# Optimization experiments

Measured on AMD Instinct MI355X. Metric: run time of the kernel, lower is better.

Reference implementation:

```python
import jax, jax.numpy as jnp
import numpy as np

NC = 10   # num_classes
H = 6     # num_heads
C = 384   # dim
HD = C // H
B = 16    # batch (non-anchor rows)
T = 197   # tokens (1 cls + 196 image)
N = T - 1
SCALE = HD ** -0.5


def _ln(x, g, b):
    mu = jnp.mean(x, -1, keepdims=True)
    var = jnp.mean(jnp.square(x - mu), -1, keepdims=True)
    return (x - mu) * jax.lax.rsqrt(var + 1e-5) * g + b


def setup_inputs() -> dict:
    key = jax.random.key(0)
    ks = jax.random.split(key, 12)
    def w(k, shape):
        return jax.random.normal(k, shape, jnp.float32) * 0.02
    return {
        "x": jax.random.normal(ks[0], (B + NC, T, C), jnp.float32),
        "Wqv": w(ks[1], (C, 2 * C)),
        "Wk": w(ks[2], (C, C)),
        "Wq_proj": w(ks[3], (C, C)), "bq_proj": jnp.zeros((C,), jnp.float32),
        "Wqk": w(ks[4], (C, C)), "Wqk2": w(ks[5], (C, C)), "Wv": w(ks[6], (C, C)),
        "Wr_proj": w(ks[7], (C, C)), "br_proj": jnp.zeros((C,), jnp.float32),
        "g1": jnp.ones((C,), jnp.float32), "b1": jnp.zeros((C,), jnp.float32),
        "g2": jnp.ones((C,), jnp.float32), "b2": jnp.zeros((C,), jnp.float32),
        "g3": jnp.ones((C,), jnp.float32), "b3": jnp.zeros((C,), jnp.float32),
        "W1": w(ks[8], (C, 4 * C)), "bm1": jnp.zeros((4 * C,), jnp.float32),
        "W2": w(ks[9], (4 * C, C)), "bm2": jnp.zeros((C,), jnp.float32),
    }


def reference(x, Wqv, Wk, Wq_proj, bq_proj, Wqk, Wqk2, Wv, Wr_proj, br_proj,
              g1, b1, g2, b2, g3, b3, W1, bm1, W2, bm2):
    xs, anchors = x[:-NC], jax.lax.stop_gradient(x[-NC:])  # anchors .detach()
    x_im, a_im = xs[:, 1:], anchors[:, 1:]                  # [B,N,C], [NC,N,C]
    x_cls, a_cls = xs[:, :1], anchors[:, :1]                # [B,1,C], [NC,1,C]

    # ---- Quoter ----
    n1x = _ln(x_cls, g1, b1)[:, 0]    # [B,C]
    n1a = _ln(a_cls, g1, b1)[:, 0]    # [NC,C]
    qv = (n1a @ Wqv).reshape(NC, 2, H, HD)
    q, v = qv[:, 0], qv[:, 1]                       # [NC,H,HD]
    k = (n1x @ Wk).reshape(B, H, HD)                # [B,H,HD]
    attn_cls = jax.nn.softmax(jnp.einsum('nhd,bhd->bnh', q, k) * SCALE, axis=1)  # [B,NC,H]
    cls_out = jnp.einsum('bnh,nhd->bhd', attn_cls, v).reshape(B, 1, C) @ Wq_proj + bq_proj

    # ---- Rectifier ----
    n2x = _ln(x_im, g2, b2)   # [B,N,C]
    n2a = _ln(a_im, g2, b2)   # [NC,N,C]
    def heads(t, W):
        return (t @ W).reshape(t.shape[0], N, H, HD).transpose(0, 2, 1, 3)
    vr = heads(n2x, Wv)        # [B,H,N,HD]
    qh = heads(n2x, Wqk)       # [B,H,N,HD]
    kh = heads(n2a, Wqk)       # [NC,H,N,HD]
    q2 = heads(n2x, Wqk2)
    k2 = heads(n2a, Wqk2)
    # left_attn = relu(-(q @ k^T) * scale), right_attn = relu((k2 @ q2^T) * scale)
    left = jax.nn.relu(-SCALE * jnp.einsum('bhnd,chmd->bchnm', qh, kh))    # [B,NC,H,N,N]
    right = jax.nn.relu(SCALE * jnp.einsum('chmd,bhnd->bchmn', k2, q2))    # [B,NC,H,N,N]
    attn = jnp.einsum('bchnm,bchmk->bchnk', left, right).transpose(0, 2, 3, 1, 4)  # [B,H,N,NC,N]
    # faithful raw reshape [B,NC,H] -> [B,H,NC] (memory reinterpretation as in torch source)
    w2 = attn_cls.reshape(B, H, NC)
    tmp = jnp.einsum('bhc,bhnck->bhnk', w2, attn)                           # [B,H,N,N]
    # faithful raw reshape [B,H,N,HD] -> [B,N,C]
    rect = jnp.einsum('bhnk,bhkd->bhnd', tmp, vr).reshape(B, N, C) @ Wr_proj + br_proj

    x_im = x_im + rect
    xx = jnp.concatenate([cls_out, x_im], axis=1)        # [B,T,C]
    hdn = _ln(xx, g3, b3)
    xx = xx + (jax.nn.gelu(hdn @ W1 + bm1, approximate=False) @ W2 + bm2)
    return jnp.concatenate([xx, anchors], axis=0)        # [B+NC,T,C]
```

## Files before the change

### kernel.cpp

```cpp
#include <hip/hip_runtime.h>
#include <hip/hip_bf16.h>
#include <math.h>

#define SCL 0.125f

typedef float f32x4 __attribute__((ext_vector_type(4)));
typedef short bf16x8 __attribute__((ext_vector_type(8)));
#define MFMA16(a, b, c) __builtin_amdgcn_mfma_f32_16x16x32_bf16((a), (b), (c), 0, 0, 0)

__device__ __forceinline__ unsigned short f2bf(float f) {
    unsigned int u = __builtin_bit_cast(unsigned int, f);
    u = (u + 0x7FFFu + ((u >> 16) & 1u)) >> 16;
    return (unsigned short)u;
}

__device__ __forceinline__ float gelu_exact(float v) {
    return 0.5f * v * (1.f + erff(v * 0.70710678118654752f));
}

template <int BF16OUT>
__global__ void ln_kernel(const float* __restrict__ x, void* __restrict__ outp,
                          const float* __restrict__ g, const float* __restrict__ bt,
                          int mode) {
    const int row = blockIdx.x;
    const int lane = threadIdx.x;
    const float* src;
    if (mode == 0)      src = x + (size_t)row * (197 * 384);
    else if (mode == 4) {
        if (row < 3136) { int b = row / 196, n = row % 196; src = x + (size_t)(b * 197 + 1 + n) * 384; }
        else { int rr = row - 3136; int b = rr / 196, n = rr % 196; src = x + (size_t)((16 + b) * 197 + 1 + n) * 384; }
    }
    else                src = x + (size_t)row * 384;

    float v[6];
    float s = 0.f, s2 = 0.f;
#pragma unroll
    for (int j = 0; j < 6; j++) {
        v[j] = src[lane + j * 64];
        s += v[j];
        s2 += v[j] * v[j];
    }
#pragma unroll
    for (int o = 32; o; o >>= 1) {
        s  += __shfl_xor(s, o);
        s2 += __shfl_xor(s2, o);
    }
    const float mu = s * (1.f / 384.f);
    const float var = s2 * (1.f / 384.f) - mu * mu;
    const float rs = 1.f / sqrtf(var + 1e-5f);
#pragma unroll
    for (int j = 0; j < 6; j++) {
        const int c = lane + j * 64;
        const float r = (v[j] - mu) * rs * g[c] + bt[c];
        if (BF16OUT) ((unsigned short*)outp)[(size_t)row * 384 + c] = f2bf(r);
        else         ((float*)outp)[(size_t)row * 384 + c] = r;
    }
}

template <int M>
__global__ void gemm_cls(const float* __restrict__ A, const float* __restrict__ B,
                         const float* __restrict__ bias, float* __restrict__ C,
                         int N, int ldc) {
    __shared__ float sA[M * 384];
    __shared__ float red[4][M][64];
    const int t = threadIdx.x;
    const int tc = t & 63, ks = t >> 6;
    const int n = blockIdx.x * 64 + tc;
    for (int e = t; e < M * 384; e += 256) sA[e] = A[e];
    __syncthreads();
    float acc[M];
#pragma unroll
    for (int m = 0; m < M; m++) acc[m] = 0.f;
    const int k0 = ks * 96;
#pragma unroll 4
    for (int k = k0; k < k0 + 96; k++) {
        const float bv = B[(size_t)k * N + n];
#pragma unroll
        for (int m = 0; m < M; m++) acc[m] += sA[m * 384 + k] * bv;
    }
#pragma unroll
    for (int m = 0; m < M; m++) red[ks][m][tc] = acc[m];
    __syncthreads();
    if (ks == 0) {
#pragma unroll
        for (int m = 0; m < M; m++) {
            float s = red[0][m][tc] + red[1][m][tc] + red[2][m][tc] + red[3][m][tc];
            if (bias) s += bias[n];
            C[(size_t)m * ldc + n] = s;
        }
    }
}

__global__ void attn_cls_kernel(const float* __restrict__ qv, const float* __restrict__ kcls,
                                float* __restrict__ aflat, float* __restrict__ cls_pre) {
    const int b = blockIdx.x;
    const int t = threadIdx.x;
    __shared__ float kb[384];
    __shared__ float pl[60];
#pragma unroll
    for (int j = 0; j < 6; j++) kb[t + j * 64] = kcls[b * 384 + t + j * 64];
    __syncthreads();
    if (t < 60) {
        const int n = t / 6, h = t % 6;
        float acc = 0.f;
        for (int d = 0; d < 64; d++) acc += qv[n * 768 + h * 64 + d] * kb[h * 64 + d];
        pl[t] = acc * SCL;
    }
    __syncthreads();
    if (t < 6) {
        float m = -1e30f;
        for (int n = 0; n < 10; n++) m = fmaxf(m, pl[n * 6 + t]);
        float p[10], sum = 0.f;
        for (int n = 0; n < 10; n++) { p[n] = expf(pl[n * 6 + t] - m); sum += p[n]; }
        const float inv = 1.f / sum;
        for (int n = 0; n < 10; n++) {
            const float pr = p[n] * inv;
            pl[n * 6 + t] = pr;
            aflat[b * 60 + n * 6 + t] = pr;
        }
    }
    __syncthreads();
#pragma unroll
    for (int j = 0; j < 6; j++) {
        const int c = t + j * 64;
        const int h = c >> 6;
        float acc = 0.f;
        for (int n = 0; n < 10; n++) acc += pl[n * 6 + h] * qv[n * 768 + 384 + c];
        cls_pre[b * 384 + c] = acc;
    }
}

__global__ void wcast_t(const float* __restrict__ W, unsigned short* __restrict__ Wt,
                        int K, int N) {
    const int n0 = blockIdx.x * 64, k0 = blockIdx.y * 64;
    __shared__ unsigned short sT[64][72];
    const int t = threadIdx.x;
    for (int e = t; e < 4096; e += 256) {
        const int k = e >> 6, n = e & 63;
        sT[n][k] = f2bf(W[(size_t)(k0 + k) * N + n0 + n]);
    }
    __syncthreads();
    for (int e = t; e < 512; e += 256) {
        const int n = e >> 3, ch = e & 7;
        *(uint4*)&Wt[(size_t)(n0 + n) * K + k0 + ch * 8] = *(uint4*)&sT[n][ch * 8];
    }
}

__global__ void wcast3(const float* __restrict__ Wa, const float* __restrict__ Wb,
                       const float* __restrict__ Wc, unsigned short* __restrict__ Wt) {
    const float* W = blockIdx.z == 0 ? Wa : (blockIdx.z == 1 ? Wb : Wc);
    unsigned short* dst = Wt + (size_t)blockIdx.z * 384 * 384;
    const int n0 = blockIdx.x * 64, k0 = blockIdx.y * 64;
    __shared__ unsigned short sT[64][72];
    const int t = threadIdx.x;
    for (int e = t; e < 4096; e += 256) {
        const int k = e >> 6, n = e & 63;
        sT[n][k] = f2bf(W[(size_t)(k0 + k) * 384 + n0 + n]);
    }
    __syncthreads();
    for (int e = t; e < 512; e += 256) {
        const int n = e >> 3, ch = e & 7;
        *(uint4*)&dst[(size_t)(n0 + n) * 384 + k0 + ch * 8] = *(uint4*)&sT[n][ch * 8];
    }
}

template <int EPI>
__launch_bounds__(256)
__global__ void gemm_mfma(const unsigned short* __restrict__ A,
                          const unsigned short* __restrict__ Bt,
                          const float* __restrict__ bias, const float* __restrict__ res,
                          void* __restrict__ Cout, int M, int N, int K) {
    const int m0 = blockIdx.y * 64, n0 = blockIdx.x * 128;
    const int t = threadIdx.x;
    const int w = t >> 6, l = t & 63;
    const int lr = l & 15, lk = l >> 4;
    const int wr = w >> 1, wc = w & 1;

    __shared__ unsigned short sA[64][72];
    __shared__ unsigned short sB[128][72];

    f32x4 acc[2][4];
#pragma unroll
    for (int mi = 0; mi < 2; mi++)
#pragma unroll
        for (int nj = 0; nj < 4; nj++) acc[mi][nj] = (f32x4){0.f, 0.f, 0.f, 0.f};

    for (int k0 = 0; k0 < K; k0 += 64) {
        for (int e = t; e < 512; e += 256) {
            const int r = e >> 3, ch = e & 7;
            uint4 v = make_uint4(0, 0, 0, 0);
            const int row = m0 + r;
            if (row < M) v = *(const uint4*)(A + (size_t)row * K + k0 + ch * 8);
            *(uint4*)&sA[r][ch * 8] = v;
        }
        for (int e = t; e < 1024; e += 256) {
            const int r = e >> 3, ch = e & 7;
            *(uint4*)&sB[r][ch * 8] = *(const uint4*)(Bt + (size_t)(n0 + r) * K + k0 + ch * 8);
        }
        __syncthreads();
#pragma unroll
        for (int kc = 0; kc < 2; kc++) {
            bf16x8 af[2], bfr[4];
#pragma unroll
            for (int mi = 0; mi < 2; mi++)
                af[mi] = *(const bf16x8*)&sA[wr * 32 + mi * 16 + lr][kc * 32 + lk * 8];
#pragma unroll
            for (int nj = 0; nj < 4; nj++)
                bfr[nj] = *(const bf16x8*)&sB[wc * 64 + nj * 16 + lr][kc * 32 + lk * 8];
#pragma unroll
            for (int mi = 0; mi < 2; mi++)
#pragma unroll
                for (int nj = 0; nj < 4; nj++)
                    acc[mi][nj] = MFMA16(af[mi], bfr[nj], acc[mi][nj]);
        }
        __syncthreads();
    }

#pragma unroll
    for (int mi = 0; mi < 2; mi++)
#pragma unroll
        for (int nj = 0; nj < 4; nj++) {
            const int col = n0 + wc * 64 + nj * 16 + lr;
#pragma unroll
            for (int i = 0; i < 4; i++) {
                const int row = m0 + wr * 32 + mi * 16 + lk * 4 + i;
                if (row >= M) continue;
                float v = acc[mi][nj][i];
                if (EPI == 0) {
                    ((unsigned short*)Cout)[(size_t)row * N + col] = f2bf(v);
                } else if (EPI == 1) {
                    const int crow = row + row / 196 + 1;
                    v += bias[col] + res[(size_t)crow * N + col];
                    ((float*)Cout)[(size_t)crow * N + col] = v;
                } else if (EPI == 2) {
                    ((unsigned short*)Cout)[(size_t)row * N + col] = f2bf(gelu_exact(v + bias[col]));
                } else {
                    v += bias[col] + res[(size_t)row * N + col];
                    ((float*)Cout)[(size_t)row * N + col] = v;
                }
            }
        }
}

__global__ __launch_bounds__(256, 2)
void rz_kernel(const unsigned short* __restrict__ Q2b, const unsigned short* __restrict__ K2b,
               const unsigned short* __restrict__ VRb, unsigned short* __restrict__ Zt,
               int sq, int sk, int sv) {
    const int c = blockIdx.x, h = blockIdx.y, b = blockIdx.z;
    const int t = threadIdx.x;
    const int w = t >> 6, l = t & 63;
    const int lr = l & 15, lk = l >> 4;

    __shared__ unsigned short sVT[64 * 232];
    __shared__ unsigned short sR[4 * 16 * 232];
    unsigned short* sRw = sR + w * (16 * 232);

    const unsigned short* vrsrc = VRb + (size_t)(b * 196) * sv + h * 64;
    for (int e = t; e < 196 * 8; e += 256) {
        const int kk = e >> 3, ch = e & 7;
        uint4 v = *(const uint4*)(vrsrc + (size_t)kk * sv + ch * 8);
        unsigned short vs[8]; *(uint4*)vs = v;
#pragma unroll
        for (int j = 0; j < 8; j++) sVT[(ch * 8 + j) * 232 + kk] = vs[j];
    }
    for (int e = t; e < 64 * 36; e += 256) sVT[(e / 36) * 232 + 196 + (e % 36)] = 0;
    for (int e = l; e < 16 * 24; e += 64) sRw[(e / 24) * 232 + 208 + (e % 24)] = 0;

    bf16x8 qf0[13], qf1[13];
    const unsigned short* q2src = Q2b + (size_t)(b * 196) * sq + h * 64;
#pragma unroll
    for (int kt = 0; kt < 13; kt++) {
        const int r = kt * 16 + lr;
        if (r < 196) {
            const unsigned short* p = q2src + (size_t)r * sq;
            qf0[kt] = *(const bf16x8*)(p + lk * 8);
            qf1[kt] = *(const bf16x8*)(p + 32 + lk * 8);
        } else {
            qf0[kt] = (bf16x8){0, 0, 0, 0, 0, 0, 0, 0};
            qf1[kt] = (bf16x8){0, 0, 0, 0, 0, 0, 0, 0};
        }
    }
    __syncthreads();

    const unsigned short* k2src = K2b + (size_t)(c * 196) * sk + h * 64;
    unsigned short* zdst = Zt + ((((size_t)(b * 6 + h)) * 10 + c) * 64) * 208;

    for (int mt = w; mt < 13; mt += 4) {
        bf16x8 a0, a1;
        const int ar = mt * 16 + lr;
        if (ar < 196) {
            const unsigned short* p = k2src + (size_t)ar * sk;
            a0 = *(const bf16x8*)(p + lk * 8);
            a1 = *(const bf16x8*)(p + 32 + lk * 8);
        } else {
            a0 = (bf16x8){0, 0, 0, 0, 0, 0, 0, 0};
            a1 = (bf16x8){0, 0, 0, 0, 0, 0, 0, 0};
        }
#pragma unroll
        for (int kt = 0; kt < 13; kt++) {
            f32x4 acc = {0.f, 0.f, 0.f, 0.f};
            acc = MFMA16(a0, qf0[kt], acc);
            acc = MFMA16(a1, qf1[kt], acc);
#pragma unroll
            for (int i = 0; i < 4; i++)
                sRw[(lk * 4 + i) * 232 + kt * 16 + lr] = f2bf(fmaxf(0.f, SCL * acc[i]));
        }
#pragma unroll
        for (int dt = 0; dt < 4; dt++) {
            f32x4 acc = {0.f, 0.f, 0.f, 0.f};
#pragma unroll
            for (int kc = 0; kc < 7; kc++) {
                bf16x8 a  = *(const bf16x8*)&sRw[lr * 232 + kc * 32 + lk * 8];
                bf16x8 bb = *(const bf16x8*)&sVT[(dt * 16 + lr) * 232 + kc * 32 + lk * 8];
                acc = MFMA16(a, bb, acc);
            }
            unsigned short p[4];
#pragma unroll
            for (int i = 0; i < 4; i++) p[i] = f2bf(acc[i]);
            *(uint2*)&zdst[(size_t)(dt * 16 + lr) * 208 + mt * 16 + lk * 4] = *(uint2*)p;
        }
    }
}

__global__ __launch_bounds__(256)
void yz_kernel(const unsigned short* __restrict__ QHb, const unsigned short* __restrict__ KHb,
               const unsigned short* __restrict__ Zt, const float* __restrict__ aflat,
               unsigned short* __restrict__ rect) {
    const int ns = blockIdx.x, h = blockIdx.y, b = blockIdx.z;
    const int n0 = ns * 49;
    const int t = threadIdx.x;
    const int w = t >> 6, l = t & 63;
    const int lr = l & 15, lk = l >> 4;

    __shared__ unsigned short sKH[112 * 72];
    __shared__ unsigned short sZT[64 * 232];
    __shared__ unsigned short sL[64 * 232];

    for (int e = t; e < 64 * 24; e += 256) {
        sZT[(e / 24) * 232 + 208 + (e % 24)] = 0;
        sL [(e / 24) * 232 + 208 + (e % 24)] = 0;
    }

    bf16x8 qf[2];
    {
        const int rel = w * 16 + lr;
        if (rel < 49) {
            const unsigned short* qsrc = QHb + (size_t)(b * 196 + n0 + rel) * 1152 + h * 64;
            qf[0] = *(const bf16x8*)(qsrc + lk * 8);
            qf[1] = *(const bf16x8*)(qsrc + 32 + lk * 8);
        } else {
            qf[0] = (bf16x8){0, 0, 0, 0, 0, 0, 0, 0};
            qf[1] = (bf16x8){0, 0, 0, 0, 0, 0, 0, 0};
        }
    }

    f32x4 y[4];
#pragma unroll
    for (int i = 0; i < 4; i++) y[i] = (f32x4){0.f, 0.f, 0.f, 0.f};
    __syncthreads();

    for (int c = 0; c < 10; c++) {
        const unsigned short* zsrc = Zt + ((((size_t)(b * 6 + h)) * 10 + c) * 64) * 208;
        for (int e = t; e < 64 * 26; e += 256) {
            const int d = e / 26, mc = e % 26;
            *(uint4*)&sZT[d * 232 + mc * 8] = *(const uint4*)(zsrc + (size_t)d * 208 + mc * 8);
        }
        for (int e = t; e < 112 * 8; e += 256) {
            const int r = e >> 3, ch = e & 7;
            *(uint4*)&sKH[r * 72 + ch * 8] =
                *(const uint4*)(KHb + (size_t)(c * 196 + r) * 768 + h * 64 + ch * 8);
        }
        const float wc = aflat[b * 60 + h * 10 + c];
        __syncthreads();
#pragma unroll
        for (int mt = 0; mt < 7; mt++) {
            f32x4 acc = {0.f, 0.f, 0.f, 0.f};
            bf16x8 b0 = *(const bf16x8*)&sKH[(mt * 16 + lr) * 72 + lk * 8];
            acc = MFMA16(qf[0], b0, acc);
            bf16x8 b1 = *(const bf16x8*)&sKH[(mt * 16 + lr) * 72 + 32 + lk * 8];
            acc = MFMA16(qf[1], b1, acc);
            const int lrow = w * 16 + lk * 4, lcol = mt * 16 + lr;
#pragma unroll
            for (int i = 0; i < 4; i++)
                sL[(lrow + i) * 232 + lcol] = f2bf(wc * fmaxf(0.f, -SCL * acc[i]));
        }
        __syncthreads();
        for (int e = t; e < 96 * 8; e += 256) {
            const int r = e >> 3, ch = e & 7;
            uint4 v = make_uint4(0, 0, 0, 0);
            if (112 + r < 196)
                v = *(const uint4*)(KHb + (size_t)(c * 196 + 112 + r) * 768 + h * 64 + ch * 8);
            *(uint4*)&sKH[r * 72 + ch * 8] = v;
        }
        __syncthreads();
#pragma unroll
        for (int mt = 7; mt < 13; mt++) {
            f32x4 acc = {0.f, 0.f, 0.f, 0.f};
            bf16x8 b0 = *(const bf16x8*)&sKH[((mt - 7) * 16 + lr) * 72 + lk * 8];
            acc = MFMA16(qf[0], b0, acc);
            bf16x8 b1 = *(const bf16x8*)&sKH[((mt - 7) * 16 + lr) * 72 + 32 + lk * 8];
            acc = MFMA16(qf[1], b1, acc);
            const int lrow = w * 16 + lk * 4, lcol = mt * 16 + lr;
#pragma unroll
            for (int i = 0; i < 4; i++)
                sL[(lrow + i) * 232 + lcol] = f2bf(wc * fmaxf(0.f, -SCL * acc[i]));
        }
#pragma unroll
        for (int dt = 0; dt < 4; dt++) {
            f32x4 acc = y[dt];
#pragma unroll
            for (int mc = 0; mc < 7; mc++) {
                bf16x8 a  = *(const bf16x8*)&sL[(w * 16 + lr) * 232 + mc * 32 + lk * 8];
                bf16x8 bb = *(const bf16x8*)&sZT[(dt * 16 + lr) * 232 + mc * 32 + lk * 8];
                acc = MFMA16(a, bb, acc);
            }
            y[dt] = acc;
        }
        __syncthreads();
    }

#pragma unroll
    for (int dt = 0; dt < 4; dt++)
#pragma unroll
        for (int i = 0; i < 4; i++) {
            const int rel = w * 16 + lk * 4 + i;
            if (rel < 49)
                rect[(((size_t)(b * 6 + h)) * 196 + n0 + rel) * 64 + dt * 16 + lr] = f2bf(y[dt][i]);
        }
}

__global__ void copy_anchors(const float* __restrict__ x, float* __restrict__ out) {
    const int e = blockIdx.x * 256 + threadIdx.x;
    if (e < 189120) {
        const int base = 16 * 197 * 384 / 4;
        ((float4*)out)[base + e] = ((const float4*)x)[base + e];
    }
}

extern "C" void kernel_launch(void* const* d_in, const int* in_sizes, int n_in,
                              void* d_out, int out_size, void* d_ws, size_t ws_size,
                              hipStream_t stream) {
    (void)in_sizes; (void)n_in; (void)out_size; (void)ws_size;
    const float* x       = (const float*)d_in[0];
    const float* Wqv     = (const float*)d_in[1];
    const float* Wk      = (const float*)d_in[2];
    const float* Wq_proj = (const float*)d_in[3];
    const float* bq_proj = (const float*)d_in[4];
    const float* Wqk     = (const float*)d_in[5];
    const float* Wqk2    = (const float*)d_in[6];
    const float* Wv      = (const float*)d_in[7];
    const float* Wr_proj = (const float*)d_in[8];
    const float* br_proj = (const float*)d_in[9];
    const float* g1      = (const float*)d_in[10];
    const float* b1      = (const float*)d_in[11];
    const float* g2      = (const float*)d_in[12];
    const float* b2      = (const float*)d_in[13];
    const float* g3      = (const float*)d_in[14];
    const float* b3      = (const float*)d_in[15];
    const float* W1      = (const float*)d_in[16];
    const float* bm1     = (const float*)d_in[17];
    const float* W2      = (const float*)d_in[18];
    const float* bm2     = (const float*)d_in[19];

    float* ws = (float*)d_ws;
    float* n1      = ws;
    float* qv      = ws + 9984;
    float* kcls    = ws + 17664;
    float* aflat   = ws + 23808;
    float* cls_pre = ws + 24768;
    unsigned short* n2x_bf  = (unsigned short*)(ws + 30912);
    unsigned short* n2a_bf  = (unsigned short*)(ws + 633024);
    unsigned short* Px      = (unsigned short*)(ws + 1009344);
    unsigned short* Pa      = (unsigned short*)(ws + 2815680);
    unsigned short* rect_bf = (unsigned short*)(ws + 3568320);
    float* xx               = ws + 4170432;
    unsigned short* Wx_t    = (unsigned short*)(ws + 5380800);
    unsigned short* Wr_t    = (unsigned short*)(ws + 5601984);
    unsigned short* W1_t    = (unsigned short*)(ws + 5675712);
    unsigned short* W2_t    = (unsigned short*)(ws + 5970624);
    unsigned short* Zt      = (unsigned short*)(ws + 6265536);
    unsigned short* hdn_bf  = (unsigned short*)(ws + 6265536);
    unsigned short* G_bf    = (unsigned short*)(ws + 6870720);
    float* outf = (float*)d_out;

    unsigned short* QHb = Px;
    unsigned short* Q2b = Px + 384;
    unsigned short* VRb = Px + 768;
    unsigned short* KHb = Pa;
    unsigned short* K2b = Pa + 384;

    wcast3<<<dim3(6, 6, 3), 256, 0, stream>>>(Wqk, Wqk2, Wv, Wx_t);
    wcast_t<<<dim3(6, 6),  256, 0, stream>>>(Wr_proj, Wr_t, 384, 384);
    wcast_t<<<dim3(24, 6), 256, 0, stream>>>(W1, W1_t, 384, 1536);
    wcast_t<<<dim3(6, 24), 256, 0, stream>>>(W2, W2_t, 1536, 384);
    ln_kernel<0><<<26, 64, 0, stream>>>(x, n1, g1, b1, 0);
    gemm_cls<10><<<12, 256, 0, stream>>>(n1 + 16 * 384, Wqv, nullptr, qv, 768, 768);
    gemm_cls<16><<<6, 256, 0, stream>>>(n1, Wk, nullptr, kcls, 384, 384);
    attn_cls_kernel<<<16, 64, 0, stream>>>(qv, kcls, aflat, cls_pre);
    ln_kernel<1><<<5096, 64, 0, stream>>>(x, n2x_bf, g2, b2, 4);
    gemm_mfma<0><<<dim3(9, 49), 256, 0, stream>>>(n2x_bf, Wx_t, nullptr, nullptr, Px, 3136, 1152, 384);
    gemm_mfma<0><<<dim3(6, 31), 256, 0, stream>>>(n2a_bf, Wx_t, nullptr, nullptr, Pa, 1960, 768, 384);
    rz_kernel<<<dim3(10, 6, 16), 256, 0, stream>>>(Q2b, K2b, VRb, Zt, 1152, 768, 1152);
    yz_kernel<<<dim3(4, 6, 16), 256, 0, stream>>>(QHb, KHb, Zt, aflat, rect_bf);
    gemm_cls<16><<<6, 256, 0, stream>>>(cls_pre, Wq_proj, bq_proj, xx, 384, 197 * 384);
    gemm_mfma<1><<<dim3(3, 49), 256, 0, stream>>>(rect_bf, Wr_t, br_proj, x, xx, 3136, 384, 384);
    ln_kernel<1><<<3152, 64, 0, stream>>>(xx, hdn_bf, g3, b3, 3);
    gemm_mfma<2><<<dim3(12, 50), 256, 0, stream>>>(hdn_bf, W1_t, bm1, nullptr, G_bf, 3152, 1536, 384);
    gemm_mfma<3><<<dim3(3, 50), 256, 0, stream>>>(G_bf, W2_t, bm2, xx, outf, 3152, 384, 1536);
    copy_anchors<<<739, 256, 0, stream>>>(x, outf);
}
```

Measured before the change: 470.1 us.

## Merge weight-cast and layernorm launches; prefetch next-class tiles in yz_kernel

Four weight-cast launches are merged into one flattened grid, and the two first-stage layernorms are merged into a single launch, cutting per-launch overhead. In yz_kernel, the Z and KH tiles for the next class are loaded into registers while the current class computes, a software-pipelining step meant to hide global-memory latency. It also adds an occupancy hint of 2 blocks per SM. The prefetch registers raise register pressure, which may conflict with that occupancy target and cause spills.

```diff
diff --git a/kernel.cpp b/kernel.cpp
--- a/kernel.cpp
+++ b/kernel.cpp
@@ -18,19 +18,23 @@
     return 0.5f * v * (1.f + erff(v * 0.70710678118654752f));
 }
 
-template <int BF16OUT>
-__global__ void ln_kernel(const float* __restrict__ x, void* __restrict__ outp,
-                          const float* __restrict__ g, const float* __restrict__ bt,
-                          int mode) {
+__global__ void ln_all(const float* __restrict__ x, float* __restrict__ n1,
+                       unsigned short* __restrict__ n2_bf,
+                       const float* __restrict__ g1, const float* __restrict__ b1,
+                       const float* __restrict__ g2, const float* __restrict__ b2) {
     const int row = blockIdx.x;
     const int lane = threadIdx.x;
     const float* src;
-    if (mode == 0)      src = x + (size_t)row * (197 * 384);
-    else if (mode == 4) {
-        if (row < 3136) { int b = row / 196, n = row % 196; src = x + (size_t)(b * 197 + 1 + n) * 384; }
-        else { int rr = row - 3136; int b = rr / 196, n = rr % 196; src = x + (size_t)((16 + b) * 197 + 1 + n) * 384; }
-    }
-    else                src = x + (size_t)row * 384;
+    const float *g, *bt;
+    if (row < 26) {
+        src = x + (size_t)row * (197 * 384);
+        g = g1; bt = b1;
+    } else {
+        const int rr = row - 26;
+        if (rr < 3136) { int b = rr / 196, n = rr % 196; src = x + (size_t)(b * 197 + 1 + n) * 384; }
+        else { int r2 = rr - 3136; int b = r2 / 196, n = r2 % 196; src = x + (size_t)((16 + b) * 197 + 1 + n) * 384; }
+        g = g2; bt = b2;
+    }
 
     float v[6];
     float s = 0.f, s2 = 0.f;
@@ -52,8 +56,36 @@
     for (int j = 0; j < 6; j++) {
         const int c = lane + j * 64;
         const float r = (v[j] - mu) * rs * g[c] + bt[c];
-        if (BF16OUT) ((unsigned short*)outp)[(size_t)row * 384 + c] = f2bf(r);
-        else         ((float*)outp)[(size_t)row * 384 + c] = r;
+        if (row < 26) n1[(size_t)row * 384 + c] = r;
+        else          n2_bf[(size_t)(row - 26) * 384 + c] = f2bf(r);
+    }
+}
+
+__global__ void ln3_kernel(const float* __restrict__ x, unsigned short* __restrict__ outp,
+                           const float* __restrict__ g, const float* __restrict__ bt) {
+    const int row = blockIdx.x;
+    const int lane = threadIdx.x;
+    const float* src = x + (size_t)row * 384;
+    float v[6];
+    float s = 0.f, s2 = 0.f;
+#pragma unroll
+    for (int j = 0; j < 6; j++) {
+        v[j] = src[lane + j * 64];
+        s += v[j];
+        s2 += v[j] * v[j];
+    }
+#pragma unroll
+    for (int o = 32; o; o >>= 1) {
+        s  += __shfl_xor(s, o);
+        s2 += __shfl_xor(s2, o);
+    }
+    const float mu = s * (1.f / 384.f);
+    const float var = s2 * (1.f / 384.f) - mu * mu;
+    const float rs = 1.f / sqrtf(var + 1e-5f);
+#pragma unroll
+    for (int j = 0; j < 6; j++) {
+        const int c = lane + j * 64;
+        outp[(size_t)row * 384 + c] = f2bf((v[j] - mu) * rs * g[c] + bt[c]);
     }
 }
 
@@ -130,9 +162,29 @@
     }
 }
 
-__global__ void wcast_t(const float* __restrict__ W, unsigned short* __restrict__ Wt,
-                        int K, int N) {
-    const int n0 = blockIdx.x * 64, k0 = blockIdx.y * 64;
+__global__ void wcast_all(const float* __restrict__ Wqk, const float* __restrict__ Wqk2,
+                          const float* __restrict__ Wv, const float* __restrict__ Wr,
+                          const float* __restrict__ W1, const float* __restrict__ W2,
+                          unsigned short* __restrict__ Wx_t, unsigned short* __restrict__ Wr_t,
+                          unsigned short* __restrict__ W1_t, unsigned short* __restrict__ W2_t) {
+    const int bid = blockIdx.x;
+    const float* W; unsigned short* dst; int K, N, nx, ky;
+    if (bid < 108) {
+        const int z = bid / 36, rem = bid % 36;
+        W = (z == 0) ? Wqk : (z == 1 ? Wqk2 : Wv);
+        dst = Wx_t + (size_t)z * 384 * 384;
+        K = 384; N = 384; nx = rem % 6; ky = rem / 6;
+    } else if (bid < 144) {
+        const int rem = bid - 108;
+        W = Wr; dst = Wr_t; K = 384; N = 384; nx = rem % 6; ky = rem / 6;
+    } else if (bid < 288) {
+        const int rem = bid - 144;
+        W = W1; dst = W1_t; K = 384; N = 1536; nx = rem % 24; ky = rem / 24;
+    } else {
+        const int rem = bid - 288;
+        W = W2; dst = W2_t; K = 1536; N = 384; nx = rem % 6; ky = rem / 6;
+    }
+    const int n0 = nx * 64, k0 = ky * 64;
     __shared__ unsigned short sT[64][72];
     const int t = threadIdx.x;
     for (int e = t; e < 4096; e += 256) {
@@ -142,25 +194,7 @@
     __syncthreads();
     for (int e = t; e < 512; e += 256) {
         const int n = e >> 3, ch = e & 7;
-        *(uint4*)&Wt[(size_t)(n0 + n) * K + k0 + ch * 8] = *(uint4*)&sT[n][ch * 8];
-    }
-}
-
-__global__ void wcast3(const float* __restrict__ Wa, const float* __restrict__ Wb,
-                       const float* __restrict__ Wc, unsigned short* __restrict__ Wt) {
-    const float* W = blockIdx.z == 0 ? Wa : (blockIdx.z == 1 ? Wb : Wc);
-    unsigned short* dst = Wt + (size_t)blockIdx.z * 384 * 384;
-    const int n0 = blockIdx.x * 64, k0 = blockIdx.y * 64;
-    __shared__ unsigned short sT[64][72];
-    const int t = threadIdx.x;
-    for (int e = t; e < 4096; e += 256) {
-        const int k = e >> 6, n = e & 63;
-        sT[n][k] = f2bf(W[(size_t)(k0 + k) * 384 + n0 + n]);
-    }
-    __syncthreads();
-    for (int e = t; e < 512; e += 256) {
-        const int n = e >> 3, ch = e & 7;
-        *(uint4*)&dst[(size_t)(n0 + n) * 384 + k0 + ch * 8] = *(uint4*)&sT[n][ch * 8];
+        *(uint4*)&dst[(size_t)(n0 + n) * K + k0 + ch * 8] = *(uint4*)&sT[n][ch * 8];
     }
 }
 
@@ -322,7 +356,7 @@
     }
 }
 
-__global__ __launch_bounds__(256)
+__global__ __launch_bounds__(256, 2)
 void yz_kernel(const unsigned short* __restrict__ QHb, const unsigned short* __restrict__ KHb,
                const unsigned short* __restrict__ Zt, const float* __restrict__ aflat,
                unsigned short* __restrict__ rect) {
@@ -354,24 +388,69 @@
         }
     }
 
+    const size_t zbase = (((size_t)(b * 6 + h)) * 10) * 64 * 208;
+
+    uint4 zt_r[7], kh1_r[4], kh2_r[3];
+
+    {
+        const unsigned short* zsrc = Zt + zbase;
+#pragma unroll
+        for (int i = 0; i < 7; i++) {
+            const int e = t + i * 256;
+            if (e < 1664) { const int d = e / 26, mc = e % 26;
+                zt_r[i] = *(const uint4*)(zsrc + (size_t)d * 208 + mc * 8); }
+        }
+#pragma unroll
+        for (int i = 0; i < 4; i++) {
+            const int e = t + i * 256;
+            if (e < 896) { const int r = e >> 3, ch = e & 7;
+                kh1_r[i] = *(const uint4*)(KHb + (size_t)r * 768 + h * 64 + ch * 8); }
+        }
+    }
+
     f32x4 y[4];
 #pragma unroll
     for (int i = 0; i < 4; i++) y[i] = (f32x4){0.f, 0.f, 0.f, 0.f};
     __syncthreads();
 
     for (int c = 0; c < 10; c++) {
-        const unsigned short* zsrc = Zt + ((((size_t)(b * 6 + h)) * 10 + c) * 64) * 208;
-        for (int e = t; e < 64 * 26; e += 256) {
-            const int d = e / 26, mc = e % 26;
-            *(uint4*)&sZT[d * 232 + mc * 8] = *(const uint4*)(zsrc + (size_t)d * 208 + mc * 8);
-        }
-        for (int e = t; e < 112 * 8; e += 256) {
+#pragma unroll
+        for (int i = 0; i < 7; i++) {
+            const int e = t + i * 256;
+            if (e < 1664) { const int d = e / 26, mc = e % 26;
+                *(uint4*)&sZT[d * 232 + mc * 8] = zt_r[i]; }
+        }
+#pragma unroll
+        for (int i = 0; i < 4; i++) {
+            const int e = t + i * 256;
+            if (e < 896) { const int r = e >> 3, ch = e & 7;
+                *(uint4*)&sKH[r * 72 + ch * 8] = kh1_r[i]; }
+        }
+#pragma unroll
+        for (int i = 0; i < 3; i++) {
+            const int e = t + i * 256;
             const int r = e >> 3, ch = e & 7;
-            *(uint4*)&sKH[r * 72 + ch * 8] =
-                *(const uint4*)(KHb + (size_t)(c * 196 + r) * 768 + h * 64 + ch * 8);
+            kh2_r[i] = (112 + r < 196)
+                ? *(const uint4*)(KHb + (size_t)(c * 196 + 112 + r) * 768 + h * 64 + ch * 8)
+                : make_uint4(0, 0, 0, 0);
         }
         const float wc = aflat[b * 60 + h * 10 + c];
         __syncthreads();
+        if (c < 9) {
+            const unsigned short* zsrc = Zt + zbase + (size_t)(c + 1) * 64 * 208;
+#pragma unroll
+            for (int i = 0; i < 7; i++) {
+                const int e = t + i * 256;
+                if (e < 1664) { const int d = e / 26, mc = e % 26;
+                    zt_r[i] = *(const uint4*)(zsrc + (size_t)d * 208 + mc * 8); }
+            }
+#pragma unroll
+            for (int i = 0; i < 4; i++) {
+                const int e = t + i * 256;
+                if (e < 896) { const int r = e >> 3, ch = e & 7;
+                    kh1_r[i] = *(const uint4*)(KHb + (size_t)((c + 1) * 196 + r) * 768 + h * 64 + ch * 8); }
+            }
+        }
 #pragma unroll
         for (int mt = 0; mt < 7; mt++) {
             f32x4 acc = {0.f, 0.f, 0.f, 0.f};
@@ -385,12 +464,11 @@
                 sL[(lrow + i) * 232 + lcol] = f2bf(wc * fmaxf(0.f, -SCL * acc[i]));
         }
         __syncthreads();
-        for (int e = t; e < 96 * 8; e += 256) {
+#pragma unroll
+        for (int i = 0; i < 3; i++) {
+            const int e = t + i * 256;
             const int r = e >> 3, ch = e & 7;
-            uint4 v = make_uint4(0, 0, 0, 0);
-            if (112 + r < 196)
-                v = *(const uint4*)(KHb + (size_t)(c * 196 + 112 + r) * 768 + h * 64 + ch * 8);
-            *(uint4*)&sKH[r * 72 + ch * 8] = v;
+            *(uint4*)&sKH[r * 72 + ch * 8] = kh2_r[i];
         }
         __syncthreads();
 #pragma unroll
@@ -489,22 +567,19 @@
     unsigned short* KHb = Pa;
     unsigned short* K2b = Pa + 384;
 
-    wcast3<<<dim3(6, 6, 3), 256, 0, stream>>>(Wqk, Wqk2, Wv, Wx_t);
-    wcast_t<<<dim3(6, 6),  256, 0, stream>>>(Wr_proj, Wr_t, 384, 384);
-    wcast_t<<<dim3(24, 6), 256, 0, stream>>>(W1, W1_t, 384, 1536);
-    wcast_t<<<dim3(6, 24), 256, 0, stream>>>(W2, W2_t, 1536, 384);
-    ln_kernel<0><<<26, 64, 0, stream>>>(x, n1, g1, b1, 0);
+    wcast_all<<<432, 256, 0, stream>>>(Wqk, Wqk2, Wv, Wr_proj, W1, W2,
+                                       Wx_t, Wr_t, W1_t, W2_t);
+    ln_all<<<5122, 64, 0, stream>>>(x, n1, n2x_bf, g1, b1, g2, b2);
     gemm_cls<10><<<12, 256, 0, stream>>>(n1 + 16 * 384, Wqv, nullptr, qv, 768, 768);
     gemm_cls<16><<<6, 256, 0, stream>>>(n1, Wk, nullptr, kcls, 384, 384);
     attn_cls_kernel<<<16, 64, 0, stream>>>(qv, kcls, aflat, cls_pre);
-    ln_kernel<1><<<5096, 64, 0, stream>>>(x, n2x_bf, g2, b2, 4);
     gemm_mfma<0><<<dim3(9, 49), 256, 0, stream>>>(n2x_bf, Wx_t, nullptr, nullptr, Px, 3136, 1152, 384);
     gemm_mfma<0><<<dim3(6, 31), 256, 0, stream>>>(n2a_bf, Wx_t, nullptr, nullptr, Pa, 1960, 768, 384);
     rz_kernel<<<dim3(10, 6, 16), 256, 0, stream>>>(Q2b, K2b, VRb, Zt, 1152, 768, 1152);
     yz_kernel<<<dim3(4, 6, 16), 256, 0, stream>>>(QHb, KHb, Zt, aflat, rect_bf);
     gemm_cls<16><<<6, 256, 0, stream>>>(cls_pre, Wq_proj, bq_proj, xx, 384, 197 * 384);
     gemm_mfma<1><<<dim3(3, 49), 256, 0, stream>>>(rect_bf, Wr_t, br_proj, x, xx, 3136, 384, 384);
-    ln_kernel<1><<<3152, 64, 0, stream>>>(xx, hdn_bf, g3, b3, 3);
+    ln3_kernel<<<3152, 64, 0, stream>>>(xx, hdn_bf, g3, b3);
     gemm_mfma<2><<<dim3(12, 50), 256, 0, stream>>>(hdn_bf, W1_t, bm1, nullptr, G_bf, 3152, 1536, 384);
     gemm_mfma<3><<<dim3(3, 50), 256, 0, stream>>>(G_bf, W2_t, bm2, xx, outf, 3152, 384, 1536);
     copy_anchors<<<739, 256, 0, stream>>>(x, outf);
```

Result: slower. 491.5 us (+4.5%).
